# Optimization experiments

Measured on AMD Instinct MI355X. Metric: run time of the kernel, lower is better.

Reference implementation:

```python
import jax, jax.numpy as jnp
import numpy as np

HASH_CODE_LEN = 8  # config['hash_code_len']
EPS = 1e-12

def _l2norm(x):
    n = jnp.sqrt(jnp.sum(x * x, axis=-1, keepdims=True))
    return x / jnp.maximum(n, EPS)

def setup_inputs() -> dict:
    key = jax.random.key(0)
    k1, k2, k3, k4 = jax.random.split(key, 4)
    B, H, S, D = 2, 12, 2048, 64
    Q = jax.random.normal(k1, (B, H, S, D), dtype=jnp.float32)
    K = jax.random.normal(k2, (B, H, S, D), dtype=jnp.float32)
    V = jax.random.normal(k3, (B, H, S, D), dtype=jnp.float32)
    mask = jnp.ones((B, S), dtype=jnp.float32)
    conv_w = jax.random.normal(k4, (H, 1, 3, 1), dtype=jnp.float32)  # depthwise Conv2d weight [H,1,w,1]
    return {"Q": Q, "K": K, "V": V, "mask": mask, "conv_w": conv_w}

def reference(Q, K, V, mask, conv_w):
    B, H, S, D = Q.shape
    # conv branch: depthwise conv over the sequence axis, per head (groups=num_head)
    Vm = V * mask[:, None, :, None]  # [B,H,S,D]
    conv_V = jax.lax.conv_general_dilated(
        Vm, conv_w,
        window_strides=(1, 1),
        padding=[(1, 1), (0, 0)],  # (conv_window//2, 0)
        dimension_numbers=("NCHW", "OIHW", "NCHW"),
        feature_group_count=H,
    )
    # YOSO attention: exact expectation of LSH cumulation.
    # collision prob of unit vectors q,k over hash_code_len bits: (1 - acos(q.k)/pi)^tau
    qn = _l2norm(Q)
    kn = _l2norm(K)
    dots = jnp.einsum("bhsd,bhtd->bhst", qn, kn)
    dots = jnp.clip(dots, -1.0, 1.0)
    W = (1.0 - jnp.arccos(dots) / jnp.pi) ** HASH_CODE_LEN  # [B,H,S,S]
    W = W * mask[:, None, None, :]  # key mask
    X = jnp.einsum("bhst,bhtd->bhsd", W, V)
    X = X * mask[:, None, :, None]  # query mask
    X = _l2norm(X)  # kernel.normalize(X)
    return X + conv_V
```

## Files before the change

### kernel.cpp

```cpp
#include <hip/hip_runtime.h>
#include <hip/hip_bf16.h>
#include <math.h>

#define NB 2
#define NH 12
#define NS 2048
#define ND 64
#define NBH (NB * NH)
#define TILE_USHORT 4096
#define QK_BLOCKS 6144
#define V_BLOCKS (NBH * 32)

typedef __attribute__((ext_vector_type(8))) short short8;
typedef __attribute__((ext_vector_type(4))) float floatx4;

__device__ __forceinline__ unsigned short f32_to_bf16_rne(float f) {
  unsigned int u = __float_as_uint(f);
  u += 0x7fffu + ((u >> 16) & 1u);
  return (unsigned short)(u >> 16);
}

__device__ __forceinline__ unsigned int pack_bf16_trunc(float lo, float hi) {
  return __builtin_amdgcn_perm(__float_as_uint(hi), __float_as_uint(lo), 0x07060302);
}

__device__ __forceinline__ void dma16(const unsigned short* g, unsigned short* l) {
  __builtin_amdgcn_global_load_lds(
      (const __attribute__((address_space(1))) void*)g,
      (__attribute__((address_space(3))) void*)l, 16, 0, 0);
}

__device__ __forceinline__ float yoso_f_exact(float d) {
  const float c0 = 0.49996030f;
  const float c1 = -0.06751822f;
  const float c2 = 0.02363774f;
  const float c3 = -0.00596174f;
  float a = fminf(fabsf(d), 1.0f);
  float p = fmaf(fmaf(fmaf(c3, a, c2), a, c1), a, c0);
  float u = sqrtf(1.0f - a) * p;
  return (d >= 0.0f) ? (1.0f - u) : u;
}

__global__ __launch_bounds__(256) void prep_all(
    const float* __restrict__ Q, const float* __restrict__ K,
    const float* __restrict__ V,
    unsigned short* __restrict__ qimg, unsigned short* __restrict__ kimg,
    unsigned short* __restrict__ vimg) {
  int blk = blockIdx.x;
  if (blk < QK_BLOCKS) {
    int row = blk * 16 + (threadIdx.x >> 4);
    int li  = threadIdx.x & 15;
    const float* src = Q;
    unsigned short* dst = qimg;
    if (row >= NBH * NS) { src = K; dst = kimg; row -= NBH * NS; }
    float4 v = *(const float4*)(src + (size_t)row * ND + li * 4);
    float ss = v.x * v.x + v.y * v.y + v.z * v.z + v.w * v.w;
    ss += __shfl_xor(ss, 1, 64);
    ss += __shfl_xor(ss, 2, 64);
    ss += __shfl_xor(ss, 4, 64);
    ss += __shfl_xor(ss, 8, 64);
    float rn = 1.0f / fmaxf(sqrtf(ss), 1e-12f);
    ushort4 o;
    o.x = f32_to_bf16_rne(v.x * rn);
    o.y = f32_to_bf16_rne(v.y * rn);
    o.z = f32_to_bf16_rne(v.z * rn);
    o.w = f32_to_bf16_rne(v.w * rn);
    int bh = row >> 11;
    int s  = row & (NS - 1);
    int kt = s >> 6, r = s & 63;
    size_t off = (size_t)(bh * 32 + kt) * TILE_USHORT +
                 r * 64 + (((li >> 1) ^ (r & 7)) * 8) + (li & 1) * 4;
    *(ushort4*)(dst + off) = o;
  } else {
    int vb = blk - QK_BLOCKS;
    int bh = vb >> 5, kt = vb & 31, t0 = kt * 64;
    __shared__ float sT[64][65];
    int tid = threadIdx.x;
    int tr = tid >> 2;
    int dc = (tid & 3) * 16;
    const float* vp = V + ((size_t)bh * NS + t0 + tr) * ND + dc;
    #pragma unroll
    for (int j = 0; j < 16; j += 4) {
      float4 v = *(const float4*)(vp + j);
      sT[dc + j + 0][tr] = v.x;
      sT[dc + j + 1][tr] = v.y;
      sT[dc + j + 2][tr] = v.z;
      sT[dc + j + 3][tr] = v.w;
    }
    __syncthreads();
    int dr = tid >> 2;
    unsigned short* op = vimg + (size_t)(bh * 32 + kt) * TILE_USHORT + dr * 64;
    #pragma unroll
    for (int g = 0; g < 4; ++g) {
      int combo = (tid & 3) * 4 + g;
      int c = combo >> 1;
      int w = combo & 1;
      int tb = 32 * (c >> 2) + 16 * w + 4 * (c & 3);
      ushort4 o;
      o.x = f32_to_bf16_rne(sT[dr][tb + 0]);
      o.y = f32_to_bf16_rne(sT[dr][tb + 1]);
      o.z = f32_to_bf16_rne(sT[dr][tb + 2]);
      o.w = f32_to_bf16_rne(sT[dr][tb + 3]);
      *(ushort4*)(op + ((c ^ (dr & 7)) * 8) + 4 * w) = o;
    }
  }
}

__global__ __launch_bounds__(256, 3) void yoso_main(
    const unsigned short* __restrict__ qimg, const unsigned short* __restrict__ kimg,
    const unsigned short* __restrict__ vimg, const float* __restrict__ V,
    const float* __restrict__ mask, const float* __restrict__ conv_w,
    float* __restrict__ out) {
  int bh = blockIdx.x >> 5;
  int b  = bh / NH;
  int h  = bh % NH;
  int qt = blockIdx.x & 31;
  int s0 = qt * 64;

  __shared__ unsigned short sK[2][TILE_USHORT];
  __shared__ unsigned short sV[2][TILE_USHORT];

  int tid  = threadIdx.x;
  int wv   = tid >> 6;
  int lane = tid & 63;
  int lq   = lane & 15;
  int quad = lane >> 4;
  int qh   = wv & 1;
  int kp   = wv >> 1;
  int swz  = lq & 7;

  uint4 qfrag[2][2];
  {
    const unsigned short* qtile = qimg + (size_t)(bh * 32 + qt) * TILE_USHORT;
    #pragma unroll
    for (int su = 0; su < 2; ++su)
      #pragma unroll
      for (int kk = 0; kk < 2; ++kk) {
        int R = qh * 32 + su * 16 + lq;
        qfrag[su][kk] = *(const uint4*)(qtile + R * 64 + (((kk * 4 + quad) ^ swz) * 8));
      }
  }

  float w0 = conv_w[h * 3 + 0], w1 = conv_w[h * 3 + 1], w2 = conv_w[h * 3 + 2];

  floatx4 acc[2][4];
  #pragma unroll
  for (int su = 0; su < 2; ++su)
    #pragma unroll
    for (int fd = 0; fd < 4; ++fd) acc[su][fd] = (floatx4){0.f, 0.f, 0.f, 0.f};

  const unsigned short* kb  = kimg + (size_t)bh * 32 * TILE_USHORT;
  const unsigned short* vbI = vimg + (size_t)bh * 32 * TILE_USHORT;

  const unsigned short* stage_g0 = (wv < 2) ? kb : vbI;
  unsigned short* stage_l = (wv < 2) ? &sK[wv & 1][0] : &sV[wv & 1][0];
  int stage_par = wv & 1;

  const float P0 = 0.3183098862f;
  const float P1 = 0.0530516477f;
  const float P2 = 0.0238732415f;
  const float P3 = 0.0142098402f;
  const float P4 = 0.0096701727f;
  const float P5 = 0.0071212906f;

  for (int ss = 0; ss < 16; ++ss) {
    __syncthreads();
    {
      const unsigned short* g =
          stage_g0 + (size_t)(ss * 2 + stage_par) * TILE_USHORT + lane * 8;
      #pragma unroll
      for (int c = 0; c < 8; ++c) dma16(g + c * 512, stage_l + c * 512);
    }
    __syncthreads();

    int kt = ss * 2 + kp;
    const unsigned short* myK = &sK[kp][0];
    const unsigned short* myV = &sV[kp][0];

    floatx4 sc[2][4];
    #pragma unroll
    for (int su = 0; su < 2; ++su)
      #pragma unroll
      for (int ft = 0; ft < 4; ++ft) sc[su][ft] = (floatx4){0.f, 0.f, 0.f, 0.f};
    #pragma unroll
    for (int kk = 0; kk < 2; ++kk) {
      short8 bk[4];
      #pragma unroll
      for (int ft = 0; ft < 4; ++ft)
        bk[ft] = *(const short8*)(myK + (ft * 16 + lq) * 64 + (((kk * 4 + quad) ^ swz) * 8));
      #pragma unroll
      for (int su = 0; su < 2; ++su) {
        short8 bq = *(const short8*)&qfrag[su][kk];
        #pragma unroll
        for (int ft = 0; ft < 4; ++ft)
          sc[su][ft] = __builtin_amdgcn_mfma_f32_16x16x32_bf16(bk[ft], bq, sc[su][ft], 0, 0, 0);
      }
    }

    const float4* mp = (const float4*)(mask + b * NS + kt * 64) + quad;
    floatx4 warr[2][4];
    float mx = 0.f;
    #pragma unroll
    for (int su = 0; su < 2; ++su)
      #pragma unroll
      for (int ft = 0; ft < 4; ++ft) {
        floatx4 a = sc[su][ft];
        mx = fmaxf(mx, fmaxf(fmaxf(fabsf(a[0]), fabsf(a[1])),
                             fmaxf(fabsf(a[2]), fabsf(a[3]))));
      }
    if (__builtin_expect(__any(mx > 0.82f), 0)) {
      #pragma unroll
      for (int ft = 0; ft < 4; ++ft) {
        float4 km4 = mp[ft * 4];
        #pragma unroll
        for (int su = 0; su < 2; ++su) {
          floatx4 wv4;
          #pragma unroll
          for (int r = 0; r < 4; ++r) {
            float f = yoso_f_exact(sc[su][ft][r]);
            float f2 = f * f;
            float f4 = f2 * f2;
            wv4[r] = f4 * f4;
          }
          wv4[0] *= km4.x; wv4[1] *= km4.y; wv4[2] *= km4.z; wv4[3] *= km4.w;
          warr[su][ft] = wv4;
        }
      }
    } else {
      #pragma unroll
      for (int ft = 0; ft < 4; ++ft) {
        float4 km4s = mp[ft * 4];
        floatx4 km4 = (floatx4){km4s.x, km4s.y, km4s.z, km4s.w};
        #pragma unroll
        for (int su = 0; su < 2; ++su) {
          floatx4 d = sc[su][ft];
          floatx4 y = d * d;
          floatx4 p = ((((P5 * y + P4) * y + P3) * y + P2) * y + P1) * y + P0;
          floatx4 f = p * d + 0.5f;
          floatx4 f2 = f * f;
          floatx4 f4 = f2 * f2;
          warr[su][ft] = f4 * f4 * km4;
        }
      }
    }

    #pragma unroll
    for (int kk2 = 0; kk2 < 2; ++kk2) {
      short8 av[4];
      #pragma unroll
      for (int fd = 0; fd < 4; ++fd)
        av[fd] = *(const short8*)(myV + (fd * 16 + lq) * 64 + (((kk2 * 4 + quad) ^ swz) * 8));
      #pragma unroll
      for (int su = 0; su < 2; ++su) {
        uint4 u;
        u.x = pack_bf16_trunc(warr[su][2 * kk2][0], warr[su][2 * kk2][1]);
        u.y = pack_bf16_trunc(warr[su][2 * kk2][2], warr[su][2 * kk2][3]);
        u.z = pack_bf16_trunc(warr[su][2 * kk2 + 1][0], warr[su][2 * kk2 + 1][1]);
        u.w = pack_bf16_trunc(warr[su][2 * kk2 + 1][2], warr[su][2 * kk2 + 1][3]);
        short8 bw = *(short8*)&u;
        #pragma unroll
        for (int fd = 0; fd < 4; ++fd)
          acc[su][fd] = __builtin_amdgcn_mfma_f32_16x16x32_bf16(av[fd], bw, acc[su][fd], 0, 0, 0);
      }
    }
  }

  __syncthreads();
  float* xch = (float*)&sK[0][0];
  {
    float* wr = xch + wv * 1024;
    #pragma unroll
    for (int fd = 0; fd < 4; ++fd)
      #pragma unroll
      for (int r = 0; r < 4; ++r)
        wr[lq * 64 + fd * 16 + quad * 4 + r] = acc[1 - kp][fd][r];
  }
  __syncthreads();
  {
    const float* rd = xch + (wv ^ 2) * 1024;
    #pragma unroll
    for (int fd = 0; fd < 4; ++fd)
      #pragma unroll
      for (int r = 0; r < 4; ++r)
        acc[kp][fd][r] += rd[lq * 64 + fd * 16 + quad * 4 + r];
  }

  int s = s0 + qh * 32 + kp * 16 + lq;
  float qm  = mask[b * NS + s];
  float qm0 = (s > 0) ? mask[b * NS + s - 1] : 0.f;
  float qm2 = (s < NS - 1) ? mask[b * NS + s + 1] : 0.f;
  float ssum = 0.f;
  #pragma unroll
  for (int fd = 0; fd < 4; ++fd)
    #pragma unroll
    for (int r = 0; r < 4; ++r) {
      float x = acc[kp][fd][r] * qm;
      acc[kp][fd][r] = x;
      ssum += x * x;
    }
  ssum += __shfl_xor(ssum, 16, 64);
  ssum += __shfl_xor(ssum, 32, 64);
  float rn = 1.0f / fmaxf(sqrtf(ssum), 1e-12f);

  const float* vfull = V + ((size_t)bh * NS + s) * ND;
  #pragma unroll
  for (int fd = 0; fd < 4; ++fd) {
    int d = fd * 16 + quad * 4;
    float4 vc1 = *(const float4*)(vfull + d);
    float4 cv;
    cv.x = w1 * vc1.x * qm; cv.y = w1 * vc1.y * qm;
    cv.z = w1 * vc1.z * qm; cv.w = w1 * vc1.w * qm;
    if (s > 0) {
      float4 vc0 = *(const float4*)(vfull - ND + d);
      cv.x += w0 * vc0.x * qm0; cv.y += w0 * vc0.y * qm0;
      cv.z += w0 * vc0.z * qm0; cv.w += w0 * vc0.w * qm0;
    }
    if (s < NS - 1) {
      float4 vc2 = *(const float4*)(vfull + ND + d);
      cv.x += w2 * vc2.x * qm2; cv.y += w2 * vc2.y * qm2;
      cv.z += w2 * vc2.z * qm2; cv.w += w2 * vc2.w * qm2;
    }
    float4 o;
    o.x = acc[kp][fd][0] * rn + cv.x;
    o.y = acc[kp][fd][1] * rn + cv.y;
    o.z = acc[kp][fd][2] * rn + cv.z;
    o.w = acc[kp][fd][3] * rn + cv.w;
    *(float4*)(out + ((size_t)bh * NS + s) * ND + d) = o;
  }
}

extern "C" void kernel_launch(void* const* d_in, const int* in_sizes, int n_in,
                              void* d_out, int out_size, void* d_ws, size_t ws_size,
                              hipStream_t stream) {
  const float* Q      = (const float*)d_in[0];
  const float* K      = (const float*)d_in[1];
  const float* V      = (const float*)d_in[2];
  const float* mask   = (const float*)d_in[3];
  const float* conv_w = (const float*)d_in[4];
  float* out = (float*)d_out;

  const size_t seg = (size_t)NBH * NS * ND * sizeof(unsigned short);
  unsigned short* qimg = (unsigned short*)d_ws;
  unsigned short* kimg = (unsigned short*)((char*)d_ws + seg);
  unsigned short* vimg = (unsigned short*)((char*)d_ws + 2 * seg);

  prep_all<<<QK_BLOCKS + V_BLOCKS, 256, 0, stream>>>(Q, K, V, qimg, kimg, vimg);
  yoso_main<<<NBH * 32, 256, 0, stream>>>(qimg, kimg, vimg, V, mask, conv_w, out);
}
```

Baseline: 149.2 us.

## Store K/V in MFMA fragment layout and load directly from global, dropping LDS staging

The prep kernel now writes Q/K/V bf16 images in a per-lane MFMA fragment order and folds the key mask into V. The main loop then reads K and V fragments straight from global memory (L2-resident) into registers instead of staging them through LDS with two barriers per iteration. The weight polynomial is evaluated with 2-wide float vectors so the compiler can emit packed FP32 math, and the reduction scratch is padded to avoid bank conflicts. This removes per-iteration synchronisation and the LDS traffic. In exchange every wave reloads its tiles from global/L2 with no cross-wave reuse, and the unroll-1 loop may expose load latency.

```diff
diff --git a/kernel.cpp b/kernel.cpp
--- a/kernel.cpp
+++ b/kernel.cpp
@@ -13,6 +13,7 @@
 
 typedef __attribute__((ext_vector_type(8))) short short8;
 typedef __attribute__((ext_vector_type(4))) float floatx4;
+typedef __attribute__((ext_vector_type(2))) float float2v;
 
 __device__ __forceinline__ unsigned short f32_to_bf16_rne(float f) {
   unsigned int u = __float_as_uint(f);
@@ -24,10 +25,12 @@
   return __builtin_amdgcn_perm(__float_as_uint(hi), __float_as_uint(lo), 0x07060302);
 }
 
-__device__ __forceinline__ void dma16(const unsigned short* g, unsigned short* l) {
-  __builtin_amdgcn_global_load_lds(
-      (const __attribute__((address_space(1))) void*)g,
-      (__attribute__((address_space(3))) void*)l, 16, 0, 0);
+__device__ __forceinline__ float2v mk2(float x) { return (float2v){x, x}; }
+__device__ __forceinline__ float2v max2(float2v a, float2v b) {
+  return (float2v){fmaxf(a[0], b[0]), fmaxf(a[1], b[1])};
+}
+__device__ __forceinline__ float2v abs2(float2v a) {
+  return (float2v){fabsf(a[0]), fabsf(a[1])};
 }
 
 __device__ __forceinline__ float yoso_f_exact(float d) {
@@ -43,7 +46,7 @@
 
 __global__ __launch_bounds__(256) void prep_all(
     const float* __restrict__ Q, const float* __restrict__ K,
-    const float* __restrict__ V,
+    const float* __restrict__ V, const float* __restrict__ mask,
     unsigned short* __restrict__ qimg, unsigned short* __restrict__ kimg,
     unsigned short* __restrict__ vimg) {
   int blk = blockIdx.x;
@@ -68,40 +71,49 @@
     int bh = row >> 11;
     int s  = row & (NS - 1);
     int kt = s >> 6, r = s & 63;
-    size_t off = (size_t)(bh * 32 + kt) * TILE_USHORT +
-                 r * 64 + (((li >> 1) ^ (r & 7)) * 8) + (li & 1) * 4;
+    int frag = (li >> 3) * 4 + (r >> 4);
+    int ln   = ((li >> 1) & 3) * 16 + (r & 15);
+    size_t off = (size_t)(bh * 32 + kt) * TILE_USHORT + frag * 512 + ln * 8 + (li & 1) * 4;
     *(ushort4*)(dst + off) = o;
   } else {
     int vb = blk - QK_BLOCKS;
     int bh = vb >> 5, kt = vb & 31, t0 = kt * 64;
+    int b  = bh / NH;
     __shared__ float sT[64][65];
     int tid = threadIdx.x;
     int tr = tid >> 2;
     int dc = (tid & 3) * 16;
+    float m = mask[b * NS + t0 + tr];
     const float* vp = V + ((size_t)bh * NS + t0 + tr) * ND + dc;
     #pragma unroll
-    for (int j = 0; j < 16; j += 4) {
-      float4 v = *(const float4*)(vp + j);
-      sT[dc + j + 0][tr] = v.x;
-      sT[dc + j + 1][tr] = v.y;
-      sT[dc + j + 2][tr] = v.z;
-      sT[dc + j + 3][tr] = v.w;
+    for (int jj = 0; jj < 16; jj += 4) {
+      float4 v = *(const float4*)(vp + jj);
+      sT[dc + jj + 0][tr] = v.x * m;
+      sT[dc + jj + 1][tr] = v.y * m;
+      sT[dc + jj + 2][tr] = v.z * m;
+      sT[dc + jj + 3][tr] = v.w * m;
     }
     __syncthreads();
     int dr = tid >> 2;
-    unsigned short* op = vimg + (size_t)(bh * 32 + kt) * TILE_USHORT + dr * 64;
-    #pragma unroll
-    for (int g = 0; g < 4; ++g) {
-      int combo = (tid & 3) * 4 + g;
-      int c = combo >> 1;
-      int w = combo & 1;
-      int tb = 32 * (c >> 2) + 16 * w + 4 * (c & 3);
-      ushort4 o;
-      o.x = f32_to_bf16_rne(sT[dr][tb + 0]);
-      o.y = f32_to_bf16_rne(sT[dr][tb + 1]);
-      o.z = f32_to_bf16_rne(sT[dr][tb + 2]);
-      o.w = f32_to_bf16_rne(sT[dr][tb + 3]);
-      *(ushort4*)(op + ((c ^ (dr & 7)) * 8) + 4 * w) = o;
+    unsigned short* op = vimg + (size_t)(bh * 32 + kt) * TILE_USHORT;
+    #pragma unroll
+    for (int g = 0; g < 2; ++g) {
+      int combo = (tid & 3) * 2 + g;
+      int kk2 = combo >> 2;
+      int qd  = combo & 3;
+      uint4 u;
+      int tb = kk2 * 32 + qd * 4;
+      u.x = (unsigned int)f32_to_bf16_rne(sT[dr][tb + 0]) |
+            ((unsigned int)f32_to_bf16_rne(sT[dr][tb + 1]) << 16);
+      u.y = (unsigned int)f32_to_bf16_rne(sT[dr][tb + 2]) |
+            ((unsigned int)f32_to_bf16_rne(sT[dr][tb + 3]) << 16);
+      u.z = (unsigned int)f32_to_bf16_rne(sT[dr][tb + 16]) |
+            ((unsigned int)f32_to_bf16_rne(sT[dr][tb + 17]) << 16);
+      u.w = (unsigned int)f32_to_bf16_rne(sT[dr][tb + 18]) |
+            ((unsigned int)f32_to_bf16_rne(sT[dr][tb + 19]) << 16);
+      int frag = kk2 * 4 + (dr >> 4);
+      int ln   = qd * 16 + (dr & 15);
+      *(uint4*)(op + frag * 512 + ln * 8) = u;
     }
   }
 }
@@ -117,8 +129,7 @@
   int qt = blockIdx.x & 31;
   int s0 = qt * 64;
 
-  __shared__ unsigned short sK[2][TILE_USHORT];
-  __shared__ unsigned short sV[2][TILE_USHORT];
+  __shared__ float xch[4 * 1088];
 
   int tid  = threadIdx.x;
   int wv   = tid >> 6;
@@ -127,7 +138,6 @@
   int quad = lane >> 4;
   int qh   = wv & 1;
   int kp   = wv >> 1;
-  int swz  = lq & 7;
 
   uint4 qfrag[2][2];
   {
@@ -135,10 +145,8 @@
     #pragma unroll
     for (int su = 0; su < 2; ++su)
       #pragma unroll
-      for (int kk = 0; kk < 2; ++kk) {
-        int R = qh * 32 + su * 16 + lq;
-        qfrag[su][kk] = *(const uint4*)(qtile + R * 64 + (((kk * 4 + quad) ^ swz) * 8));
-      }
+      for (int kk = 0; kk < 2; ++kk)
+        qfrag[su][kk] = *(const uint4*)(qtile + (kk * 4 + qh * 2 + su) * 512 + lane * 8);
   }
 
   float w0 = conv_w[h * 3 + 0], w1 = conv_w[h * 3 + 1], w2 = conv_w[h * 3 + 2];
@@ -151,10 +159,6 @@
 
   const unsigned short* kb  = kimg + (size_t)bh * 32 * TILE_USHORT;
   const unsigned short* vbI = vimg + (size_t)bh * 32 * TILE_USHORT;
-
-  const unsigned short* stage_g0 = (wv < 2) ? kb : vbI;
-  unsigned short* stage_l = (wv < 2) ? &sK[wv & 1][0] : &sV[wv & 1][0];
-  int stage_par = wv & 1;
 
   const float P0 = 0.3183098862f;
   const float P1 = 0.0530516477f;
@@ -163,19 +167,18 @@
   const float P4 = 0.0096701727f;
   const float P5 = 0.0071212906f;
 
+  #pragma unroll 1
   for (int ss = 0; ss < 16; ++ss) {
-    __syncthreads();
-    {
-      const unsigned short* g =
-          stage_g0 + (size_t)(ss * 2 + stage_par) * TILE_USHORT + lane * 8;
-      #pragma unroll
-      for (int c = 0; c < 8; ++c) dma16(g + c * 512, stage_l + c * 512);
-    }
-    __syncthreads();
-
     int kt = ss * 2 + kp;
-    const unsigned short* myK = &sK[kp][0];
-    const unsigned short* myV = &sV[kp][0];
+    const unsigned short* ktile = kb  + (size_t)kt * TILE_USHORT;
+    const unsigned short* vtile = vbI + (size_t)kt * TILE_USHORT;
+
+    uint4 kf[2][4];
+    #pragma unroll
+    for (int kk = 0; kk < 2; ++kk)
+      #pragma unroll
+      for (int ft = 0; ft < 4; ++ft)
+        kf[kk][ft] = *(const uint4*)(ktile + (kk * 4 + ft) * 512 + lane * 8);
 
     floatx4 sc[2][4];
     #pragma unroll
@@ -183,106 +186,101 @@
       #pragma unroll
       for (int ft = 0; ft < 4; ++ft) sc[su][ft] = (floatx4){0.f, 0.f, 0.f, 0.f};
     #pragma unroll
-    for (int kk = 0; kk < 2; ++kk) {
-      short8 bk[4];
-      #pragma unroll
-      for (int ft = 0; ft < 4; ++ft)
-        bk[ft] = *(const short8*)(myK + (ft * 16 + lq) * 64 + (((kk * 4 + quad) ^ swz) * 8));
+    for (int kk = 0; kk < 2; ++kk)
       #pragma unroll
       for (int su = 0; su < 2; ++su) {
         short8 bq = *(const short8*)&qfrag[su][kk];
         #pragma unroll
         for (int ft = 0; ft < 4; ++ft)
-          sc[su][ft] = __builtin_amdgcn_mfma_f32_16x16x32_bf16(bk[ft], bq, sc[su][ft], 0, 0, 0);
+          sc[su][ft] = __builtin_amdgcn_mfma_f32_16x16x32_bf16(
+              *(const short8*)&kf[kk][ft], bq, sc[su][ft], 0, 0, 0);
       }
-    }
-
-    const float4* mp = (const float4*)(mask + b * NS + kt * 64) + quad;
-    floatx4 warr[2][4];
-    float mx = 0.f;
-    #pragma unroll
-    for (int su = 0; su < 2; ++su)
-      #pragma unroll
-      for (int ft = 0; ft < 4; ++ft) {
-        floatx4 a = sc[su][ft];
-        mx = fmaxf(mx, fmaxf(fmaxf(fabsf(a[0]), fabsf(a[1])),
-                             fmaxf(fabsf(a[2]), fabsf(a[3]))));
+
+    uint4 vf[2][4];
+    #pragma unroll
+    for (int kk2 = 0; kk2 < 2; ++kk2)
+      #pragma unroll
+      for (int fd = 0; fd < 4; ++fd)
+        vf[kk2][fd] = *(const uint4*)(vtile + (kk2 * 4 + fd) * 512 + lane * 8);
+
+    {
+      float2v mxy = mk2(0.f);
+      #pragma unroll
+      for (int su = 0; su < 2; ++su)
+        #pragma unroll
+        for (int ft = 0; ft < 4; ++ft) {
+          float2v* p = (float2v*)&sc[su][ft];
+          mxy = max2(mxy, max2(abs2(p[0]), abs2(p[1])));
+        }
+      float mx = fmaxf(mxy[0], mxy[1]);
+      if (__builtin_expect(__any(mx > 0.82f), 0)) {
+        #pragma unroll
+        for (int su = 0; su < 2; ++su)
+          #pragma unroll
+          for (int ft = 0; ft < 4; ++ft)
+            #pragma unroll
+            for (int r = 0; r < 4; ++r) {
+              float f = yoso_f_exact(sc[su][ft][r]);
+              float f2 = f * f;
+              float f4 = f2 * f2;
+              sc[su][ft][r] = f4 * f4;
+            }
+      } else {
+        float2v c5 = mk2(P5), c4 = mk2(P4), c3 = mk2(P3), c2 = mk2(P2),
+                c1 = mk2(P1), c0 = mk2(P0), hf = mk2(0.5f);
+        #pragma unroll
+        for (int su = 0; su < 2; ++su)
+          #pragma unroll
+          for (int ft = 0; ft < 4; ++ft) {
+            float2v* p = (float2v*)&sc[su][ft];
+            #pragma unroll
+            for (int hh = 0; hh < 2; ++hh) {
+              float2v d = p[hh];
+              float2v y = d * d;
+              float2v pp = ((((c5 * y + c4) * y + c3) * y + c2) * y + c1) * y + c0;
+              float2v f = pp * d + hf;
+              float2v f2 = f * f;
+              float2v f4 = f2 * f2;
+              p[hh] = f4 * f4;
+            }
+          }
       }
-    if (__builtin_expect(__any(mx > 0.82f), 0)) {
-      #pragma unroll
-      for (int ft = 0; ft < 4; ++ft) {
-        float4 km4 = mp[ft * 4];
-        #pragma unroll
-        for (int su = 0; su < 2; ++su) {
-          floatx4 wv4;
-          #pragma unroll
-          for (int r = 0; r < 4; ++r) {
-            float f = yoso_f_exact(sc[su][ft][r]);
-            float f2 = f * f;
-            float f4 = f2 * f2;
-            wv4[r] = f4 * f4;
-          }
-          wv4[0] *= km4.x; wv4[1] *= km4.y; wv4[2] *= km4.z; wv4[3] *= km4.w;
-          warr[su][ft] = wv4;
-        }
-      }
-    } else {
-      #pragma unroll
-      for (int ft = 0; ft < 4; ++ft) {
-        float4 km4s = mp[ft * 4];
-        floatx4 km4 = (floatx4){km4s.x, km4s.y, km4s.z, km4s.w};
-        #pragma unroll
-        for (int su = 0; su < 2; ++su) {
-          floatx4 d = sc[su][ft];
-          floatx4 y = d * d;
-          floatx4 p = ((((P5 * y + P4) * y + P3) * y + P2) * y + P1) * y + P0;
-          floatx4 f = p * d + 0.5f;
-          floatx4 f2 = f * f;
-          floatx4 f4 = f2 * f2;
-          warr[su][ft] = f4 * f4 * km4;
-        }
-      }
-    }
-
-    #pragma unroll
-    for (int kk2 = 0; kk2 < 2; ++kk2) {
-      short8 av[4];
-      #pragma unroll
-      for (int fd = 0; fd < 4; ++fd)
-        av[fd] = *(const short8*)(myV + (fd * 16 + lq) * 64 + (((kk2 * 4 + quad) ^ swz) * 8));
+    }
+
+    #pragma unroll
+    for (int kk2 = 0; kk2 < 2; ++kk2)
       #pragma unroll
       for (int su = 0; su < 2; ++su) {
         uint4 u;
-        u.x = pack_bf16_trunc(warr[su][2 * kk2][0], warr[su][2 * kk2][1]);
-        u.y = pack_bf16_trunc(warr[su][2 * kk2][2], warr[su][2 * kk2][3]);
-        u.z = pack_bf16_trunc(warr[su][2 * kk2 + 1][0], warr[su][2 * kk2 + 1][1]);
-        u.w = pack_bf16_trunc(warr[su][2 * kk2 + 1][2], warr[su][2 * kk2 + 1][3]);
+        u.x = pack_bf16_trunc(sc[su][2 * kk2][0], sc[su][2 * kk2][1]);
+        u.y = pack_bf16_trunc(sc[su][2 * kk2][2], sc[su][2 * kk2][3]);
+        u.z = pack_bf16_trunc(sc[su][2 * kk2 + 1][0], sc[su][2 * kk2 + 1][1]);
+        u.w = pack_bf16_trunc(sc[su][2 * kk2 + 1][2], sc[su][2 * kk2 + 1][3]);
         short8 bw = *(short8*)&u;
         #pragma unroll
         for (int fd = 0; fd < 4; ++fd)
-          acc[su][fd] = __builtin_amdgcn_mfma_f32_16x16x32_bf16(av[fd], bw, acc[su][fd], 0, 0, 0);
+          acc[su][fd] = __builtin_amdgcn_mfma_f32_16x16x32_bf16(
+              *(const short8*)&vf[kk2][fd], bw, acc[su][fd], 0, 0, 0);
       }
-    }
-  }
-
-  __syncthreads();
-  float* xch = (float*)&sK[0][0];
-  {
-    float* wr = xch + wv * 1024;
-    #pragma unroll
-    for (int fd = 0; fd < 4; ++fd)
-      #pragma unroll
-      for (int r = 0; r < 4; ++r)
-        wr[lq * 64 + fd * 16 + quad * 4 + r] = acc[1 - kp][fd][r];
-  }
+  }
+
   __syncthreads();
   {
-    const float* rd = xch + (wv ^ 2) * 1024;
+    float* wr = xch + wv * 1088;
     #pragma unroll
     for (int fd = 0; fd < 4; ++fd)
       #pragma unroll
       for (int r = 0; r < 4; ++r)
-        acc[kp][fd][r] += rd[lq * 64 + fd * 16 + quad * 4 + r];
+        wr[lq * 68 + fd * 16 + quad * 4 + r] = acc[1 - kp][fd][r];
+  }
+  __syncthreads();
+  {
+    const float* rd = xch + (wv ^ 2) * 1088;
+    #pragma unroll
+    for (int fd = 0; fd < 4; ++fd)
+      #pragma unroll
+      for (int r = 0; r < 4; ++r)
+        acc[kp][fd][r] += rd[lq * 68 + fd * 16 + quad * 4 + r];
   }
 
   int s = s0 + qh * 32 + kp * 16 + lq;
@@ -344,6 +342,6 @@
   unsigned short* kimg = (unsigned short*)((char*)d_ws + seg);
   unsigned short* vimg = (unsigned short*)((char*)d_ws + 2 * seg);
 
-  prep_all<<<QK_BLOCKS + V_BLOCKS, 256, 0, stream>>>(Q, K, V, qimg, kimg, vimg);
+  prep_all<<<QK_BLOCKS + V_BLOCKS, 256, 0, stream>>>(Q, K, V, mask, qimg, kimg, vimg);
   yoso_main<<<NBH * 32, 256, 0, stream>>>(qimg, kimg, vimg, V, mask, conv_w, out);
 }
```

After: 151.3 us. Within noise of the previous version (+1.4%).
